# Performance work log

Measured on AMD Instinct MI355X. Metric: run time of the kernel, lower is better.

The kernel has to match this reference:

```python
import jax, jax.numpy as jnp
import numpy as np

N = 50000
E = 500000
C = 128
NUM_TYPES = 32
DIM_TOK = 94
STEPS = 3
BLOCKS = 2
NUM_ET = 3
LN_EPS = 1e-5


def setup_inputs() -> dict:
    key = jax.random.key(0)
    ks = jax.random.split(key, 16)
    s = 0.05
    return {
        "x_type": jax.random.randint(ks[0], (N,), 0, NUM_TYPES),
        "x_tok": jax.random.randint(ks[1], (N,), 0, DIM_TOK),
        "x_small": jax.random.normal(ks[2], (N, 2), jnp.float32),
        "edge_index": jax.random.randint(ks[3], (2, E), 0, N),
        "edge_type": jax.random.randint(ks[4], (E,), 0, NUM_ET),
        "conv_w": jax.random.normal(ks[5], (BLOCKS, NUM_ET, STEPS, C, C), jnp.float32) * s,
        "gru_wih": jax.random.normal(ks[6], (BLOCKS, NUM_ET, 3 * C, C), jnp.float32) * s,
        "gru_whh": jax.random.normal(ks[7], (BLOCKS, NUM_ET, 3 * C, C), jnp.float32) * s,
        "gru_bih": jnp.zeros((BLOCKS, NUM_ET, 3 * C), jnp.float32),
        "gru_bhh": jnp.zeros((BLOCKS, NUM_ET, 3 * C), jnp.float32),
        "ln_g": jnp.ones((BLOCKS, C), jnp.float32),
        "ln_b": jnp.zeros((BLOCKS, C), jnp.float32),
        "head_w1": jax.random.normal(ks[8], (C, C), jnp.float32) * s,
        "head_b1": jnp.zeros((C,), jnp.float32),
        "head_w2": jax.random.normal(ks[9], (2, C), jnp.float32) * s,
        "head_b2": jnp.zeros((2,), jnp.float32),
    }


def _gru_cell(x, h, wih, whh, bih, bhh):
    # torch.nn.GRUCell: gates ordered (r, z, n)
    gi = x @ wih.T + bih  # [N, 3C]
    gh = h @ whh.T + bhh
    gi_r, gi_z, gi_n = jnp.split(gi, 3, axis=-1)
    gh_r, gh_z, gh_n = jnp.split(gh, 3, axis=-1)
    r = jax.nn.sigmoid(gi_r + gh_r)
    z = jax.nn.sigmoid(gi_z + gh_z)
    n = jnp.tanh(gi_n + r * gh_n)
    return (1.0 - z) * n + z * h


def _forward(x_small, conv_w, gru_wih, gru_whh, gru_bih, gru_bhh, ln_g, ln_b,
             head_w1, head_b1, head_w2, head_b2, x_type, x_tok, edge_index, edge_type):
    # build_features: one-hot type, one-hot (clamped) token, small feats
    h_type = jax.nn.one_hot(x_type, NUM_TYPES, dtype=x_small.dtype)
    h_tok = jax.nn.one_hot(jnp.clip(x_tok, 0, DIM_TOK - 1), DIM_TOK, dtype=x_small.dtype)
    h = jnp.concatenate([h_type, h_tok, x_small], axis=1)  # [N, C]

    src, dst = edge_index[0], edge_index[1]

    for b in range(BLOCKS):
        total = jnp.zeros_like(h)
        for t in range(NUM_ET):
            # edge-type masking implemented as weighted scatter-add (sum aggr)
            em = (edge_type == t).astype(h.dtype)[:, None]  # [E, 1]
            m = h
            for s in range(STEPS):
                x = m @ conv_w[b, t, s]                     # [N, C]
                agg = jax.ops.segment_sum(x[src] * em, dst, num_segments=N)
                m = _gru_cell(agg, m,
                              gru_wih[b, t], gru_whh[b, t],
                              gru_bih[b, t], gru_bhh[b, t])
            total = total + m
        # LayerNorm(residual) + ReLU; dropout=0 (eval)
        hr = h + total
        mu = jnp.mean(hr, axis=-1, keepdims=True)
        var = jnp.var(hr, axis=-1, keepdims=True)
        h = (hr - mu) * jax.lax.rsqrt(var + LN_EPS) * ln_g[b] + ln_b[b]
        h = jax.nn.relu(h)

    # head applied per-node (module returns head(h), not head(pooled))
    z = jax.nn.relu(h @ head_w1.T + head_b1)
    return z @ head_w2.T + head_b2  # [N, 2]


def reference(x_type, x_tok, x_small, edge_index, edge_type, conv_w, gru_wih, gru_whh,
              gru_bih, gru_bhh, ln_g, ln_b, head_w1, head_b1, head_w2, head_b2):
    return _forward(x_small, conv_w, gru_wih, gru_whh, gru_bih, gru_bhh, ln_g, ln_b,
                    head_w1, head_b1, head_w2, head_b2, x_type, x_tok, edge_index, edge_type)
```

## Files before the change

kernel.cpp:

```cpp
#include <hip/hip_runtime.h>
#include <cstdint>
#include <cstddef>

#define N_NODES 50000
#define N_EDGES 500000
#define NB 782
#define NT 150000
#define NCHUNK2 586
#define FS 49152
#define PSTR 136
#define MAXOFF 12799744u
#define ECAP 1024

typedef _Float16 half8 __attribute__((ext_vector_type(8)));
typedef _Float16 half2v __attribute__((ext_vector_type(2)));
typedef float floatx4 __attribute__((ext_vector_type(4)));

__device__ __forceinline__ float sigmoid_(float x) { return 1.f / (1.f + __expf(-x)); }
__device__ __forceinline__ float tanh_(float x) {
  float t = __expf(-2.f * fabsf(x));
  float r = (1.f - t) / (1.f + t);
  return copysignf(r, x);
}

__global__ __launch_bounds__(256) void k_feat_hist(_Float16* __restrict__ h,
    const int* __restrict__ xtype, const int* __restrict__ xtok,
    const float* __restrict__ xs, const int* __restrict__ ei,
    const int* __restrict__ et, int* __restrict__ counts) {
  int idx = blockIdx.x * 256 + threadIdx.x;
  if (idx < N_NODES * 128) {
    int n = idx >> 7, c = idx & 127;
    float v;
    if (c < 32) {
      v = (xtype[n] == c) ? 1.f : 0.f;
    } else if (c < 126) {
      int tk = xtok[n];
      tk = tk < 0 ? 0 : (tk > 93 ? 93 : tk);
      v = (tk == (c - 32)) ? 1.f : 0.f;
    } else {
      v = xs[n * 2 + (c - 126)];
    }
    h[idx] = (_Float16)v;
  }
  if (idx < N_EDGES) {
    int d = ei[N_EDGES + idx];
    int ty = et[idx] & 3;
    if ((unsigned)d < N_NODES && ty < 3) atomicAdd(&counts[ty * N_NODES + d], 1);
  }
}

__global__ __launch_bounds__(256) void k_scan_a(const int* __restrict__ counts,
    int* __restrict__ bsum) {
  int i = blockIdx.x * 256 + threadIdx.x;
  int v = (i < NT) ? counts[i] : 0;
  int lane = threadIdx.x & 63, wv = threadIdx.x >> 6;
#pragma unroll
  for (int off = 32; off > 0; off >>= 1) v += __shfl_xor(v, off);
  __shared__ int ws[4];
  if (lane == 0) ws[wv] = v;
  __syncthreads();
  if (threadIdx.x == 0) bsum[blockIdx.x] = ws[0] + ws[1] + ws[2] + ws[3];
}

__global__ __launch_bounds__(256) void k_scan_c(const int* __restrict__ counts,
    const int* __restrict__ bsum, int* __restrict__ ptr, int* __restrict__ fill) {
  __shared__ int wsum2[4];
  __shared__ int ws[4];
  int lane = threadIdx.x & 63, wv = threadIdx.x >> 6;
  int acc = 0;
  for (int j = threadIdx.x; j < blockIdx.x; j += 256) acc += bsum[j];
#pragma unroll
  for (int off = 32; off > 0; off >>= 1) acc += __shfl_xor(acc, off);
  if (lane == 0) wsum2[wv] = acc;
  __syncthreads();
  int boffset = wsum2[0] + wsum2[1] + wsum2[2] + wsum2[3];
  int i = blockIdx.x * 256 + threadIdx.x;
  int v = (i < NT) ? counts[i] : 0;
  int s = v;
#pragma unroll
  for (int off = 1; off < 64; off <<= 1) { int u = __shfl_up(s, off); if (lane >= off) s += u; }
  if (lane == 63) ws[wv] = s;
  __syncthreads();
  int woff = 0;
#pragma unroll
  for (int w = 0; w < 4; ++w) woff += (w < wv) ? ws[w] : 0;
  int excl = boffset + woff + s - v;
  if (i < NT) { ptr[i] = excl; fill[i] = excl; }
  if (blockIdx.x == NCHUNK2 - 1 && threadIdx.x == 0)
    ptr[NT] = boffset + bsum[NCHUNK2 - 1];
}

__global__ __launch_bounds__(256) void k_place(const int* __restrict__ ei,
    const int* __restrict__ et, int* __restrict__ fill, int* __restrict__ csr) {
  int e = blockIdx.x * 256 + threadIdx.x;
  if (e >= N_EDGES) return;
  int srcv = ei[e], d = ei[N_EDGES + e], ty = et[e] & 3;
  if ((unsigned)d >= N_NODES || (unsigned)srcv >= N_NODES || ty >= 3) return;
  int pos = atomicAdd(&fill[ty * N_NODES + d], 1);
  if ((unsigned)pos < N_EDGES) csr[pos] = srcv << 8;
}

#define PREP_B (6 * 4 * 24 * 512)
#define PREP_MISC_BLOCKS ((PREP_B + 16384 + 511) / 512)
__global__ __launch_bounds__(512) void k_prep(const float* __restrict__ cw,
    const float* __restrict__ wih, const float* __restrict__ whh,
    const float* __restrict__ hw1, _Float16* __restrict__ dcomb,
    _Float16* __restrict__ dwhh, _Float16* __restrict__ dw1) {
  if (blockIdx.x < 36) {
    int mat = blockIdx.x >> 1, half = blockIdx.x & 1;
    int bt = mat / 3;
    int u = threadIdx.x >> 6, lane = threadIdx.x & 63;
    int quad = lane >> 4, l16 = lane & 15;
    floatx4 zero = {0.f, 0.f, 0.f, 0.f};
    floatx4 acc[4][3];
#pragma unroll
    for (int rt = 0; rt < 4; ++rt)
#pragma unroll
      for (int cc = 0; cc < 3; ++cc) acc[rt][cc] = zero;
#pragma unroll
    for (int jc = 0; jc < 4; ++jc) {
      half8 af[4], bf[3];
#pragma unroll
      for (int rt = 0; rt < 4; ++rt) {
        int m = half * 64 + rt * 16 + l16;
        const float* ap = cw + ((size_t)mat * 128 + m) * 128 + jc * 32 + quad * 8;
        floatx4 a0 = *(const floatx4*)ap;
        floatx4 a1 = *(const floatx4*)(ap + 4);
#pragma unroll
        for (int i = 0; i < 4; ++i) { af[rt][i] = (_Float16)a0[i]; af[rt][4 + i] = (_Float16)a1[i]; }
      }
#pragma unroll
      for (int cc = 0; cc < 3; ++cc) {
        int n = (u * 3 + cc) * 16 + l16;
        const float* bp = wih + ((size_t)bt * 384 + n) * 128 + jc * 32 + quad * 8;
        floatx4 b0 = *(const floatx4*)bp;
        floatx4 b1 = *(const floatx4*)(bp + 4);
#pragma unroll
        for (int i = 0; i < 4; ++i) { bf[cc][i] = (_Float16)b0[i]; bf[cc][4 + i] = (_Float16)b1[i]; }
      }
#pragma unroll
      for (int rt = 0; rt < 4; ++rt)
#pragma unroll
        for (int cc = 0; cc < 3; ++cc)
          acc[rt][cc] = __builtin_amdgcn_mfma_f32_16x16x32_f16(af[rt], bf[cc], acc[rt][cc], 0, 0, 0);
    }
#pragma unroll
    for (int rt = 0; rt < 4; ++rt) {
#pragma unroll
      for (int cc = 0; cc < 3; ++cc) {
        int ctg = u * 3 + cc;
#pragma unroll
        for (int q = 0; q < 4; ++q) {
          int k = half * 64 + rt * 16 + quad * 4 + q;
          int kc2 = k >> 5, r5 = k & 31;
          int lane2 = (r5 >> 3) * 16 + l16, j2 = r5 & 7;
          dcomb[(size_t)mat * FS + (size_t)((kc2 * 24 + ctg) * 64 + lane2) * 8 + j2] =
              (_Float16)acc[rt][cc][q];
        }
      }
    }
  } else {
    int idx0 = (blockIdx.x - 36) * 512 + threadIdx.x;
    if (idx0 < PREP_B) {
      int idx = idx0;
      int j = idx & 7, lane = (idx >> 3) & 63;
      int r = idx >> 9;
      int ct = r % 24;
      int r2 = r / 24;
      int kc = r2 & 3, bt = r2 >> 2;
      int k = kc * 32 + ((lane >> 4) & 3) * 8 + j;
      int n = ct * 16 + (lane & 15);
      dwhh[idx] = (_Float16)whh[((size_t)bt * 384 + n) * 128 + k];
    } else if (idx0 < PREP_B + 16384) {
      int idx = idx0 - PREP_B;
      int j = idx & 7, lane = (idx >> 3) & 63, ct = (idx >> 9) & 7, kc = (idx >> 12) & 3;
      int k = kc * 32 + ((lane >> 4) & 3) * 8 + j;
      int n = ct * 16 + (lane & 15);
      dw1[idx] = (_Float16)hw1[n * 128 + k];
    }
  }
}

__global__ __launch_bounds__(512, 4) void k_step(
    const _Float16* __restrict__ Mbase, const size_t mstride,
    _Float16* __restrict__ Sout,
    const int* __restrict__ ptr, const int* __restrict__ csr,
    const _Float16* __restrict__ WPC, const _Float16* __restrict__ WHH,
    const float* __restrict__ bi2, const float* __restrict__ bh2) {
  __shared__ __attribute__((aligned(16))) _Float16 Plds[64 * PSTR];
  __shared__ __attribute__((aligned(16))) _Float16 Mlds[64 * PSTR];
  __shared__ int Elds[ECAP];
  __shared__ int Pt[65];
  int bid = blockIdx.x;
  int t = bid / NB, blk = bid - t * NB;
  int tid = threadIdx.x;
  int wave = tid >> 6, lane = tid & 63;
  int quad = lane >> 4, l16 = lane & 15;
  int rowbase = blk * 64;
  const size_t NC = (size_t)N_NODES * 128;
  const _Float16* Mp = Mbase + mstride * t;
  const char* Mb = (const char*)Mp;
  _Float16* Sp = Sout + (size_t)t * NC;
  const int* ptrT = ptr + t * N_NODES;

  int rb64 = rowbase + 64; if (rb64 > N_NODES) rb64 = N_NODES;
  int bse = ptrT[rowbase];
  int cend = ptrT[rb64];
  if (bse < 0) bse = 0; if (bse > N_EDGES) bse = N_EDGES;
  if (cend < bse) cend = bse; if (cend > N_EDGES) cend = N_EDGES;
  int cnt = cend - bse; if (cnt > ECAP) cnt = ECAP;

  if (tid < 65) {
    int n = rowbase + tid; if (n > N_NODES) n = N_NODES;
    int v = ptrT[n] - bse;
    if (v < 0) v = 0; if (v > cnt) v = cnt;
    Pt[tid] = v;
  }
#pragma unroll
  for (int it = 0; it < 2; ++it) {
    int r = it * 32 + (tid >> 4);
    int c = (tid & 15) * 8;
    int gr = rowbase + r; if (gr >= N_NODES) gr = N_NODES - 1;
    half8 v = *(const half8*)(Mp + (size_t)gr * 128 + c);
    *(half8*)(&Mlds[r * PSTR + c]) = v;
  }
  for (int i = tid; i < cnt; i += 512) {
    unsigned off = (unsigned)csr[bse + i];
    if (off > MAXOFF) off = 0;
    Elds[i] = (int)off;
  }
  __syncthreads();

  int g = quad;
  unsigned coff = (unsigned)(l16 * 16);
  int nlA = wave * 8 + g, nlB = nlA + 4;
  int iA = Pt[nlA], eA = Pt[nlA + 1];
  int iB = Pt[nlB], eB = Pt[nlB + 1];
  half8 accA = {}, accB = {};
  while (__any(iA < eA || iB < eB)) {
#pragma unroll
    for (int uu = 0; uu < 4; ++uu) {
      if (iA + uu < eA) {
        unsigned o = (unsigned)Elds[iA + uu] + coff;
        accA += *(const half8*)(Mb + o);
      }
      if (iB + uu < eB) {
        unsigned o = (unsigned)Elds[iB + uu] + coff;
        accB += *(const half8*)(Mb + o);
      }
    }
    iA += 4; iB += 4;
  }
  *(half8*)(&Plds[nlA * PSTR + l16 * 8]) = accA;
  *(half8*)(&Plds[nlB * PSTR + l16 * 8]) = accB;
  __syncthreads();

  const half8* wpc = (const half8*)(WPC + (size_t)t * 3 * FS);
  const half8* whh = (const half8*)(WHH + (size_t)t * FS);
  const float* bi = bi2 + (size_t)t * 384;
  const float* bh = bh2 + (size_t)t * 384;
  int u = wave;
  floatx4 zero = {0.f, 0.f, 0.f, 0.f};
  floatx4 aR[4], aZ[4], aNP[4], aNM[4];
#pragma unroll
  for (int rt = 0; rt < 4; ++rt) { aR[rt] = zero; aZ[rt] = zero; aNP[rt] = zero; aNM[rt] = zero; }
#pragma unroll
  for (int kc = 0; kc < 4; ++kc) {
    half8 af[4];
#pragma unroll
    for (int rt = 0; rt < 4; ++rt)
      af[rt] = *(const half8*)(&Plds[(rt * 16 + l16) * PSTR + kc * 32 + quad * 8]);
    half8 br = wpc[(kc * 24 + u) * 64 + lane];
    half8 bz = wpc[(kc * 24 + 8 + u) * 64 + lane];
    half8 bn = wpc[(kc * 24 + 16 + u) * 64 + lane];
#pragma unroll
    for (int rt = 0; rt < 4; ++rt) {
      aR[rt] = __builtin_amdgcn_mfma_f32_16x16x32_f16(af[rt], br, aR[rt], 0, 0, 0);
      aZ[rt] = __builtin_amdgcn_mfma_f32_16x16x32_f16(af[rt], bz, aZ[rt], 0, 0, 0);
      aNP[rt] = __builtin_amdgcn_mfma_f32_16x16x32_f16(af[rt], bn, aNP[rt], 0, 0, 0);
    }
  }
#pragma unroll
  for (int kc = 0; kc < 4; ++kc) {
    half8 af[4];
#pragma unroll
    for (int rt = 0; rt < 4; ++rt)
      af[rt] = *(const half8*)(&Mlds[(rt * 16 + l16) * PSTR + kc * 32 + quad * 8]);
    half8 br = whh[(kc * 24 + u) * 64 + lane];
    half8 bz = whh[(kc * 24 + 8 + u) * 64 + lane];
    half8 bn = whh[(kc * 24 + 16 + u) * 64 + lane];
#pragma unroll
    for (int rt = 0; rt < 4; ++rt) {
      aR[rt] = __builtin_amdgcn_mfma_f32_16x16x32_f16(af[rt], br, aR[rt], 0, 0, 0);
      aZ[rt] = __builtin_amdgcn_mfma_f32_16x16x32_f16(af[rt], bz, aZ[rt], 0, 0, 0);
      aNM[rt] = __builtin_amdgcn_mfma_f32_16x16x32_f16(af[rt], bn, aNM[rt], 0, 0, 0);
    }
  }
  __syncthreads();
  int col = u * 16 + l16;
  float br_ = bi[col] + bh[col];
  float bz_ = bi[128 + col] + bh[128 + col];
  float bin = bi[256 + col], bhn = bh[256 + col];
#pragma unroll
  for (int rt = 0; rt < 4; ++rt) {
#pragma unroll
    for (int q = 0; q < 4; ++q) {
      int lr = rt * 16 + quad * 4 + q;
      float r = sigmoid_(aR[rt][q] + br_);
      float z = sigmoid_(aZ[rt][q] + bz_);
      float nt = tanh_(aNP[rt][q] + bin + r * (aNM[rt][q] + bhn));
      float hold = (float)Mlds[lr * PSTR + col];
      Plds[lr * PSTR + col] = (_Float16)((1.f - z) * nt + z * hold);
    }
  }
  __syncthreads();
#pragma unroll
  for (int it = 0; it < 2; ++it) {
    int r = it * 32 + (tid >> 4);
    int c = (tid & 15) * 8;
    int row = rowbase + r;
    if (row < N_NODES)
      *(half8*)(Sp + (size_t)row * 128 + c) = *(const half8*)(&Plds[r * PSTR + c]);
  }
}

__global__ __launch_bounds__(256) void k_ln16(_Float16* __restrict__ h,
    const _Float16* __restrict__ S, const float* __restrict__ gamma,
    const float* __restrict__ beta) {
  int wave = threadIdx.x >> 6, lane = threadIdx.x & 63;
  int g = lane >> 4, l16 = lane & 15;
  int row = blockIdx.x * 16 + wave * 4 + g;
  if (row >= N_NODES) return;
  const size_t NC = (size_t)N_NODES * 128;
  size_t base = (size_t)row * 128 + l16 * 8;
  half8 hv = *(const half8*)(h + base);
  half8 s0 = *(const half8*)(S + base);
  half8 s1 = *(const half8*)(S + NC + base);
  half8 s2 = *(const half8*)(S + 2 * NC + base);
  float v[8];
  float s = 0.f, sq = 0.f;
#pragma unroll
  for (int i = 0; i < 8; ++i) {
    v[i] = (float)hv[i] + (float)s0[i] + (float)s1[i] + (float)s2[i];
    s += v[i]; sq += v[i] * v[i];
  }
#pragma unroll
  for (int off = 1; off < 16; off <<= 1) {
    s += __shfl_xor(s, off);
    sq += __shfl_xor(sq, off);
  }
  float mu = s * 0.0078125f;
  float var = sq * 0.0078125f - mu * mu;
  float rs = rsqrtf(var + 1e-5f);
  half8 ov;
#pragma unroll
  for (int i = 0; i < 8; ++i) {
    float o = (v[i] - mu) * rs * gamma[l16 * 8 + i] + beta[l16 * 8 + i];
    ov[i] = (_Float16)fmaxf(o, 0.f);
  }
  *(half8*)(h + base) = ov;
}

__global__ __launch_bounds__(256, 4) void k_head(const _Float16* __restrict__ h,
    const _Float16* __restrict__ S, const float* __restrict__ gamma,
    const float* __restrict__ beta, const _Float16* __restrict__ Wf,
    const float* __restrict__ bias, const float* __restrict__ w2,
    const float* __restrict__ b2, float* __restrict__ out) {
  __shared__ __attribute__((aligned(16))) _Float16 zA[64 * PSTR];
  __shared__ __attribute__((aligned(16))) _Float16 zB[64 * PSTR];
  __shared__ float w2s[256];
  int wave = threadIdx.x >> 6, lane = threadIdx.x & 63;
  int quad = lane >> 4, l16 = lane & 15;
  int rowbase = blockIdx.x * 64;
  const size_t NC = (size_t)N_NODES * 128;
  w2s[threadIdx.x] = w2[threadIdx.x];
#pragma unroll
  for (int pass = 0; pass < 4; ++pass) {
    int rl = pass * 16 + wave * 4 + quad;
    int row = rowbase + rl; if (row >= N_NODES) row = N_NODES - 1;
    size_t base = (size_t)row * 128 + l16 * 8;
    half8 hv = *(const half8*)(h + base);
    half8 s0 = *(const half8*)(S + base);
    half8 s1 = *(const half8*)(S + NC + base);
    half8 s2 = *(const half8*)(S + 2 * NC + base);
    float v[8];
    float s = 0.f, sq = 0.f;
#pragma unroll
    for (int i = 0; i < 8; ++i) {
      v[i] = (float)hv[i] + (float)s0[i] + (float)s1[i] + (float)s2[i];
      s += v[i]; sq += v[i] * v[i];
    }
#pragma unroll
    for (int off = 1; off < 16; off <<= 1) {
      s += __shfl_xor(s, off);
      sq += __shfl_xor(sq, off);
    }
    float mu = s * 0.0078125f;
    float var = sq * 0.0078125f - mu * mu;
    float rs = rsqrtf(var + 1e-5f);
    half8 ov;
#pragma unroll
    for (int i = 0; i < 8; ++i) {
      float o = (v[i] - mu) * rs * gamma[l16 * 8 + i] + beta[l16 * 8 + i];
      ov[i] = (_Float16)fmaxf(o, 0.f);
    }
    *(half8*)(&zA[rl * PSTR + l16 * 8]) = ov;
  }
  __syncthreads();
  const half8* wf = (const half8*)Wf;
  floatx4 zero = {0.f, 0.f, 0.f, 0.f};
  floatx4 acc[4][2];
#pragma unroll
  for (int rt = 0; rt < 4; ++rt) { acc[rt][0] = zero; acc[rt][1] = zero; }
#pragma unroll
  for (int kc = 0; kc < 4; ++kc) {
    half8 af[4];
#pragma unroll
    for (int rt = 0; rt < 4; ++rt)
      af[rt] = *(const half8*)(&zA[(rt * 16 + l16) * PSTR + kc * 32 + quad * 8]);
    half8 b0 = wf[(kc * 8 + 2 * wave) * 64 + lane];
    half8 b1 = wf[(kc * 8 + 2 * wave + 1) * 64 + lane];
#pragma unroll
    for (int rt = 0; rt < 4; ++rt) {
      acc[rt][0] = __builtin_amdgcn_mfma_f32_16x16x32_f16(af[rt], b0, acc[rt][0], 0, 0, 0);
      acc[rt][1] = __builtin_amdgcn_mfma_f32_16x16x32_f16(af[rt], b1, acc[rt][1], 0, 0, 0);
    }
  }
  int col = wave * 32 + l16;
#pragma unroll
  for (int rt = 0; rt < 4; ++rt) {
#pragma unroll
    for (int q = 0; q < 4; ++q) {
      int lr = rt * 16 + quad * 4 + q;
      zB[lr * PSTR + col] = (_Float16)fmaxf(acc[rt][0][q] + bias[col], 0.f);
      zB[lr * PSTR + col + 16] = (_Float16)fmaxf(acc[rt][1][q] + bias[col + 16], 0.f);
    }
  }
  __syncthreads();
  int tid = threadIdx.x;
  if (tid < 128) {
    int lr = tid >> 1, o = tid & 1;
    int row = rowbase + lr;
    if (row < N_NODES) {
      const float* wr = w2s + o * 128;
      float a = 0.f;
#pragma unroll
      for (int k = 0; k < 128; ++k) a += (float)zB[lr * PSTR + k] * wr[k];
      out[(size_t)row * 2 + o] = a + b2[o];
    }
  }
}

extern "C" void kernel_launch(void* const* d_in, const int* in_sizes, int n_in,
                              void* d_out, int out_size, void* d_ws, size_t ws_size,
                              hipStream_t stream) {
  const int*   x_type  = (const int*)d_in[0];
  const int*   x_tok   = (const int*)d_in[1];
  const float* x_small = (const float*)d_in[2];
  const int*   eidx    = (const int*)d_in[3];
  const int*   etype   = (const int*)d_in[4];
  const float* conv_w  = (const float*)d_in[5];
  const float* gwih    = (const float*)d_in[6];
  const float* gwhh    = (const float*)d_in[7];
  const float* gbih    = (const float*)d_in[8];
  const float* gbhh    = (const float*)d_in[9];
  const float* ln_g    = (const float*)d_in[10];
  const float* ln_b    = (const float*)d_in[11];
  const float* hw1     = (const float*)d_in[12];
  const float* hb1     = (const float*)d_in[13];
  const float* hw2     = (const float*)d_in[14];
  const float* hb2     = (const float*)d_in[15];
  float* out = (float*)d_out;

  const size_t NC = (size_t)N_NODES * 128;
  char* W = (char*)d_ws;
  size_t off = 0;
  _Float16* h16 = (_Float16*)(W + off);     off += NC * 2;
  _Float16* S0  = (_Float16*)(W + off);     off += 3 * NC * 2;
  _Float16* S1  = (_Float16*)(W + off);     off += 3 * NC * 2;
  int* counts = (int*)(W + off);            off += (size_t)NT * 4;
  int* ptrv   = (int*)(W + off);            off += (size_t)(NT + 1) * 4;
  int* fill   = (int*)(W + off);            off += (size_t)NT * 4;
  int* bsum   = (int*)(W + off);            off += (NCHUNK2 + 1) * 4;
  int* csr    = (int*)(W + off);            off += (size_t)N_EDGES * 4;
  _Float16* WPC = (_Float16*)(W + off);     off += (size_t)18 * FS * 2;
  _Float16* WHH = (_Float16*)(W + off);     off += (size_t)6 * FS * 2;
  _Float16* W1F = (_Float16*)(W + off);     off += (size_t)16384 * 2;

  hipMemsetAsync(counts, 0, (size_t)NT * 4, stream);
  k_feat_hist<<<(N_NODES * 128 + 255) / 256, 256, 0, stream>>>(
      h16, x_type, x_tok, x_small, eidx, etype, counts);
  k_scan_a<<<NCHUNK2, 256, 0, stream>>>(counts, bsum);
  k_scan_c<<<NCHUNK2, 256, 0, stream>>>(counts, bsum, ptrv, fill);
  k_place<<<(N_EDGES + 255) / 256, 256, 0, stream>>>(eidx, etype, fill, csr);
  k_prep<<<36 + PREP_MISC_BLOCKS, 512, 0, stream>>>(
      conv_w, gwih, gwhh, hw1, WPC, WHH, W1F);

  for (int b = 0; b < 2; ++b) {
    for (int s = 0; s < 3; ++s) {
      const _Float16* Msrc = (s == 0) ? h16 : ((s == 1) ? S0 : S1);
      size_t mstr = (s == 0) ? 0 : NC;
      _Float16* Sout = (s == 1) ? S1 : S0;
      k_step<<<3 * NB, 512, 0, stream>>>(Msrc, mstr, Sout, ptrv, csr,
          WPC + (size_t)(b * 9 + s) * FS, WHH + (size_t)b * 3 * FS,
          gbih + (size_t)b * 3 * 384, gbhh + (size_t)b * 3 * 384);
    }
    if (b == 0)
      k_ln16<<<(N_NODES + 15) / 16, 256, 0, stream>>>(h16, S0, ln_g, ln_b);
  }
  k_head<<<NB, 256, 0, stream>>>(h16, S0, ln_g + 128, ln_b + 128,
                                 W1F, hb1, hw2, hb2, out);
}
```

Measured before the change: 673.1 us.

## Fuse LayerNorm and head into last GRU step via last-block-done counters

The final step kernel of each block now uses a per-row-tile atomic counter so that the last of the three edge-type blocks to finish a 64-row tile performs the LayerNorm (block 0) or LayerNorm plus MLP head (block 1) for that tile. This removes two separate kernel launches and their reads of h and the three S buffers from a cold pass, overlapping the epilogue with other tiles' step work. It adds threadfences, atomics and a memset of counters, and duplicates the step kernel code.

```diff
diff --git a/kernel.cpp b/kernel.cpp
--- a/kernel.cpp
+++ b/kernel.cpp
@@ -180,6 +180,7 @@
     }
   }
 }
+
 
 __global__ __launch_bounds__(512, 4) void k_step(
     const _Float16* __restrict__ Mbase, const size_t mstride,
@@ -324,129 +325,424 @@
   }
 }
 
-__global__ __launch_bounds__(256) void k_ln16(_Float16* __restrict__ h,
-    const _Float16* __restrict__ S, const float* __restrict__ gamma,
-    const float* __restrict__ beta) {
-  int wave = threadIdx.x >> 6, lane = threadIdx.x & 63;
-  int g = lane >> 4, l16 = lane & 15;
-  int row = blockIdx.x * 16 + wave * 4 + g;
-  if (row >= N_NODES) return;
+__global__ __launch_bounds__(512, 4) void k_step_ln(
+    const _Float16* __restrict__ Mbase, const size_t mstride,
+    _Float16* __restrict__ Sout,
+    const int* __restrict__ ptr, const int* __restrict__ csr,
+    const _Float16* __restrict__ WPC, const _Float16* __restrict__ WHH,
+    const float* __restrict__ bi2, const float* __restrict__ bh2,
+    _Float16* __restrict__ hbuf, const float* __restrict__ gamma,
+    const float* __restrict__ beta, int* __restrict__ fincnt) {
+  __shared__ __attribute__((aligned(16))) _Float16 Plds[64 * PSTR];
+  __shared__ __attribute__((aligned(16))) _Float16 Mlds[64 * PSTR];
+  __shared__ int Elds[ECAP];
+  __shared__ int Pt[65];
+  __shared__ int dofin;
+  int bid = blockIdx.x;
+  int t = bid / NB, blk = bid - t * NB;
+  int tid = threadIdx.x;
+  int wave = tid >> 6, lane = tid & 63;
+  int quad = lane >> 4, l16 = lane & 15;
+  int rowbase = blk * 64;
   const size_t NC = (size_t)N_NODES * 128;
-  size_t base = (size_t)row * 128 + l16 * 8;
-  half8 hv = *(const half8*)(h + base);
-  half8 s0 = *(const half8*)(S + base);
-  half8 s1 = *(const half8*)(S + NC + base);
-  half8 s2 = *(const half8*)(S + 2 * NC + base);
-  float v[8];
-  float s = 0.f, sq = 0.f;
-#pragma unroll
-  for (int i = 0; i < 8; ++i) {
-    v[i] = (float)hv[i] + (float)s0[i] + (float)s1[i] + (float)s2[i];
-    s += v[i]; sq += v[i] * v[i];
-  }
-#pragma unroll
-  for (int off = 1; off < 16; off <<= 1) {
-    s += __shfl_xor(s, off);
-    sq += __shfl_xor(sq, off);
-  }
-  float mu = s * 0.0078125f;
-  float var = sq * 0.0078125f - mu * mu;
-  float rs = rsqrtf(var + 1e-5f);
-  half8 ov;
-#pragma unroll
-  for (int i = 0; i < 8; ++i) {
-    float o = (v[i] - mu) * rs * gamma[l16 * 8 + i] + beta[l16 * 8 + i];
-    ov[i] = (_Float16)fmaxf(o, 0.f);
-  }
-  *(half8*)(h + base) = ov;
-}
-
-__global__ __launch_bounds__(256, 4) void k_head(const _Float16* __restrict__ h,
-    const _Float16* __restrict__ S, const float* __restrict__ gamma,
-    const float* __restrict__ beta, const _Float16* __restrict__ Wf,
-    const float* __restrict__ bias, const float* __restrict__ w2,
-    const float* __restrict__ b2, float* __restrict__ out) {
-  __shared__ __attribute__((aligned(16))) _Float16 zA[64 * PSTR];
-  __shared__ __attribute__((aligned(16))) _Float16 zB[64 * PSTR];
-  __shared__ float w2s[256];
-  int wave = threadIdx.x >> 6, lane = threadIdx.x & 63;
-  int quad = lane >> 4, l16 = lane & 15;
-  int rowbase = blockIdx.x * 64;
-  const size_t NC = (size_t)N_NODES * 128;
-  w2s[threadIdx.x] = w2[threadIdx.x];
-#pragma unroll
-  for (int pass = 0; pass < 4; ++pass) {
-    int rl = pass * 16 + wave * 4 + quad;
-    int row = rowbase + rl; if (row >= N_NODES) row = N_NODES - 1;
-    size_t base = (size_t)row * 128 + l16 * 8;
-    half8 hv = *(const half8*)(h + base);
-    half8 s0 = *(const half8*)(S + base);
-    half8 s1 = *(const half8*)(S + NC + base);
-    half8 s2 = *(const half8*)(S + 2 * NC + base);
-    float v[8];
-    float s = 0.f, sq = 0.f;
-#pragma unroll
-    for (int i = 0; i < 8; ++i) {
-      v[i] = (float)hv[i] + (float)s0[i] + (float)s1[i] + (float)s2[i];
-      s += v[i]; sq += v[i] * v[i];
-    }
-#pragma unroll
-    for (int off = 1; off < 16; off <<= 1) {
-      s += __shfl_xor(s, off);
-      sq += __shfl_xor(sq, off);
-    }
-    float mu = s * 0.0078125f;
-    float var = sq * 0.0078125f - mu * mu;
-    float rs = rsqrtf(var + 1e-5f);
-    half8 ov;
-#pragma unroll
-    for (int i = 0; i < 8; ++i) {
-      float o = (v[i] - mu) * rs * gamma[l16 * 8 + i] + beta[l16 * 8 + i];
-      ov[i] = (_Float16)fmaxf(o, 0.f);
-    }
-    *(half8*)(&zA[rl * PSTR + l16 * 8]) = ov;
-  }
-  __syncthreads();
-  const half8* wf = (const half8*)Wf;
+  const _Float16* Mp = Mbase + mstride * t;
+  const char* Mb = (const char*)Mp;
+  _Float16* Sp = Sout + (size_t)t * NC;
+  const int* ptrT = ptr + t * N_NODES;
+
+  int rb64 = rowbase + 64; if (rb64 > N_NODES) rb64 = N_NODES;
+  int bse = ptrT[rowbase];
+  int cend = ptrT[rb64];
+  if (bse < 0) bse = 0; if (bse > N_EDGES) bse = N_EDGES;
+  if (cend < bse) cend = bse; if (cend > N_EDGES) cend = N_EDGES;
+  int cnt = cend - bse; if (cnt > ECAP) cnt = ECAP;
+
+  if (tid < 65) {
+    int n = rowbase + tid; if (n > N_NODES) n = N_NODES;
+    int v = ptrT[n] - bse;
+    if (v < 0) v = 0; if (v > cnt) v = cnt;
+    Pt[tid] = v;
+  }
+#pragma unroll
+  for (int it = 0; it < 2; ++it) {
+    int r = it * 32 + (tid >> 4);
+    int c = (tid & 15) * 8;
+    int gr = rowbase + r; if (gr >= N_NODES) gr = N_NODES - 1;
+    half8 v = *(const half8*)(Mp + (size_t)gr * 128 + c);
+    *(half8*)(&Mlds[r * PSTR + c]) = v;
+  }
+  for (int i = tid; i < cnt; i += 512) {
+    unsigned off = (unsigned)csr[bse + i];
+    if (off > MAXOFF) off = 0;
+    Elds[i] = (int)off;
+  }
+  __syncthreads();
+
+  int g = quad;
+  unsigned coff = (unsigned)(l16 * 16);
+  int nlA = wave * 8 + g, nlB = nlA + 4;
+  int iA = Pt[nlA], eA = Pt[nlA + 1];
+  int iB = Pt[nlB], eB = Pt[nlB + 1];
+  half8 accA = {}, accB = {};
+  while (__any(iA < eA || iB < eB)) {
+#pragma unroll
+    for (int uu = 0; uu < 4; ++uu) {
+      if (iA + uu < eA) {
+        unsigned o = (unsigned)Elds[iA + uu] + coff;
+        accA += *(const half8*)(Mb + o);
+      }
+      if (iB + uu < eB) {
+        unsigned o = (unsigned)Elds[iB + uu] + coff;
+        accB += *(const half8*)(Mb + o);
+      }
+    }
+    iA += 4; iB += 4;
+  }
+  *(half8*)(&Plds[nlA * PSTR + l16 * 8]) = accA;
+  *(half8*)(&Plds[nlB * PSTR + l16 * 8]) = accB;
+  __syncthreads();
+
+  const half8* wpc = (const half8*)(WPC + (size_t)t * 3 * FS);
+  const half8* whh = (const half8*)(WHH + (size_t)t * FS);
+  const float* bi = bi2 + (size_t)t * 384;
+  const float* bh = bh2 + (size_t)t * 384;
+  int u = wave;
   floatx4 zero = {0.f, 0.f, 0.f, 0.f};
-  floatx4 acc[4][2];
-#pragma unroll
-  for (int rt = 0; rt < 4; ++rt) { acc[rt][0] = zero; acc[rt][1] = zero; }
+  floatx4 aR[4], aZ[4], aNP[4], aNM[4];
+#pragma unroll
+  for (int rt = 0; rt < 4; ++rt) { aR[rt] = zero; aZ[rt] = zero; aNP[rt] = zero; aNM[rt] = zero; }
 #pragma unroll
   for (int kc = 0; kc < 4; ++kc) {
     half8 af[4];
 #pragma unroll
     for (int rt = 0; rt < 4; ++rt)
-      af[rt] = *(const half8*)(&zA[(rt * 16 + l16) * PSTR + kc * 32 + quad * 8]);
-    half8 b0 = wf[(kc * 8 + 2 * wave) * 64 + lane];
-    half8 b1 = wf[(kc * 8 + 2 * wave + 1) * 64 + lane];
+      af[rt] = *(const half8*)(&Plds[(rt * 16 + l16) * PSTR + kc * 32 + quad * 8]);
+    half8 br = wpc[(kc * 24 + u) * 64 + lane];
+    half8 bz = wpc[(kc * 24 + 8 + u) * 64 + lane];
+    half8 bn = wpc[(kc * 24 + 16 + u) * 64 + lane];
 #pragma unroll
     for (int rt = 0; rt < 4; ++rt) {
-      acc[rt][0] = __builtin_amdgcn_mfma_f32_16x16x32_f16(af[rt], b0, acc[rt][0], 0, 0, 0);
-      acc[rt][1] = __builtin_amdgcn_mfma_f32_16x16x32_f16(af[rt], b1, acc[rt][1], 0, 0, 0);
-    }
-  }
-  int col = wave * 32 + l16;
+      aR[rt] = __builtin_amdgcn_mfma_f32_16x16x32_f16(af[rt], br, aR[rt], 0, 0, 0);
+      aZ[rt] = __builtin_amdgcn_mfma_f32_16x16x32_f16(af[rt], bz, aZ[rt], 0, 0, 0);
+      aNP[rt] = __builtin_amdgcn_mfma_f32_16x16x32_f16(af[rt], bn, aNP[rt], 0, 0, 0);
+    }
+  }
+#pragma unroll
+  for (int kc = 0; kc < 4; ++kc) {
+    half8 af[4];
+#pragma unroll
+    for (int rt = 0; rt < 4; ++rt)
+      af[rt] = *(const half8*)(&Mlds[(rt * 16 + l16) * PSTR + kc * 32 + quad * 8]);
+    half8 br = whh[(kc * 24 + u) * 64 + lane];
+    half8 bz = whh[(kc * 24 + 8 + u) * 64 + lane];
+    half8 bn = whh[(kc * 24 + 16 + u) * 64 + lane];
+#pragma unroll
+    for (int rt = 0; rt < 4; ++rt) {
+      aR[rt] = __builtin_amdgcn_mfma_f32_16x16x32_f16(af[rt], br, aR[rt], 0, 0, 0);
+      aZ[rt] = __builtin_amdgcn_mfma_f32_16x16x32_f16(af[rt], bz, aZ[rt], 0, 0, 0);
+      aNM[rt] = __builtin_amdgcn_mfma_f32_16x16x32_f16(af[rt], bn, aNM[rt], 0, 0, 0);
+    }
+  }
+  __syncthreads();
+  int col = u * 16 + l16;
+  float br_ = bi[col] + bh[col];
+  float bz_ = bi[128 + col] + bh[128 + col];
+  float bin = bi[256 + col], bhn = bh[256 + col];
 #pragma unroll
   for (int rt = 0; rt < 4; ++rt) {
 #pragma unroll
     for (int q = 0; q < 4; ++q) {
       int lr = rt * 16 + quad * 4 + q;
-      zB[lr * PSTR + col] = (_Float16)fmaxf(acc[rt][0][q] + bias[col], 0.f);
-      zB[lr * PSTR + col + 16] = (_Float16)fmaxf(acc[rt][1][q] + bias[col + 16], 0.f);
-    }
-  }
-  __syncthreads();
+      float r = sigmoid_(aR[rt][q] + br_);
+      float z = sigmoid_(aZ[rt][q] + bz_);
+      float nt = tanh_(aNP[rt][q] + bin + r * (aNM[rt][q] + bhn));
+      float hold = (float)Mlds[lr * PSTR + col];
+      Plds[lr * PSTR + col] = (_Float16)((1.f - z) * nt + z * hold);
+    }
+  }
+  __syncthreads();
+#pragma unroll
+  for (int it = 0; it < 2; ++it) {
+    int r = it * 32 + (tid >> 4);
+    int c = (tid & 15) * 8;
+    int row = rowbase + r;
+    if (row < N_NODES)
+      *(half8*)(Sp + (size_t)row * 128 + c) = *(const half8*)(&Plds[r * PSTR + c]);
+  }
+  __threadfence();
+  __syncthreads();
+  if (tid == 0) dofin = (atomicAdd(&fincnt[blk], 1) == 2) ? 1 : 0;
+  __syncthreads();
+  if (dofin) {
+    __threadfence();
+    int l16b = tid & 15;
+#pragma unroll
+    for (int pass = 0; pass < 2; ++pass) {
+      int rl = pass * 32 + (tid >> 4);
+      int row = rowbase + rl;
+      int rowc = row < N_NODES ? row : N_NODES - 1;
+      size_t base = (size_t)rowc * 128 + l16b * 8;
+      half8 hv = *(const half8*)(hbuf + base);
+      half8 s0 = *(const half8*)(Sout + base);
+      half8 s1 = *(const half8*)(Sout + NC + base);
+      half8 s2 = *(const half8*)(Sout + 2 * NC + base);
+      float v[8];
+      float s = 0.f, sq = 0.f;
+#pragma unroll
+      for (int i = 0; i < 8; ++i) {
+        v[i] = (float)hv[i] + (float)s0[i] + (float)s1[i] + (float)s2[i];
+        s += v[i]; sq += v[i] * v[i];
+      }
+#pragma unroll
+      for (int off = 1; off < 16; off <<= 1) {
+        s += __shfl_xor(s, off);
+        sq += __shfl_xor(sq, off);
+      }
+      float mu = s * 0.0078125f;
+      float var = sq * 0.0078125f - mu * mu;
+      float rs = rsqrtf(var + 1e-5f);
+      half8 ov;
+#pragma unroll
+      for (int i = 0; i < 8; ++i) {
+        float o = (v[i] - mu) * rs * gamma[l16b * 8 + i] + beta[l16b * 8 + i];
+        ov[i] = (_Float16)fmaxf(o, 0.f);
+      }
+      if (row < N_NODES) *(half8*)(hbuf + base) = ov;
+    }
+  }
+}
+
+__global__ __launch_bounds__(512, 4) void k_step_hd(
+    const _Float16* __restrict__ Mbase, const size_t mstride,
+    _Float16* __restrict__ Sout,
+    const int* __restrict__ ptr, const int* __restrict__ csr,
+    const _Float16* __restrict__ WPC, const _Float16* __restrict__ WHH,
+    const float* __restrict__ bi2, const float* __restrict__ bh2,
+    const _Float16* __restrict__ hbuf, const float* __restrict__ gamma,
+    const float* __restrict__ beta, int* __restrict__ fincnt,
+    const _Float16* __restrict__ W1f, const float* __restrict__ hb1,
+    const float* __restrict__ w2, const float* __restrict__ b2,
+    float* __restrict__ out) {
+  __shared__ __attribute__((aligned(16))) _Float16 Plds[64 * PSTR];
+  __shared__ __attribute__((aligned(16))) _Float16 Mlds[64 * PSTR];
+  __shared__ int Elds[ECAP];
+  __shared__ int Pt[65];
+  __shared__ int dofin;
+  int bid = blockIdx.x;
+  int t = bid / NB, blk = bid - t * NB;
   int tid = threadIdx.x;
-  if (tid < 128) {
-    int lr = tid >> 1, o = tid & 1;
-    int row = rowbase + lr;
-    if (row < N_NODES) {
-      const float* wr = w2s + o * 128;
-      float a = 0.f;
-#pragma unroll
-      for (int k = 0; k < 128; ++k) a += (float)zB[lr * PSTR + k] * wr[k];
-      out[(size_t)row * 2 + o] = a + b2[o];
+  int wave = tid >> 6, lane = tid & 63;
+  int quad = lane >> 4, l16 = lane & 15;
+  int rowbase = blk * 64;
+  const size_t NC = (size_t)N_NODES * 128;
+  const _Float16* Mp = Mbase + mstride * t;
+  const char* Mb = (const char*)Mp;
+  _Float16* Sp = Sout + (size_t)t * NC;
+  const int* ptrT = ptr + t * N_NODES;
+
+  int rb64 = rowbase + 64; if (rb64 > N_NODES) rb64 = N_NODES;
+  int bse = ptrT[rowbase];
+  int cend = ptrT[rb64];
+  if (bse < 0) bse = 0; if (bse > N_EDGES) bse = N_EDGES;
+  if (cend < bse) cend = bse; if (cend > N_EDGES) cend = N_EDGES;
+  int cnt = cend - bse; if (cnt > ECAP) cnt = ECAP;
+
+  if (tid < 65) {
+    int n = rowbase + tid; if (n > N_NODES) n = N_NODES;
+    int v = ptrT[n] - bse;
+    if (v < 0) v = 0; if (v > cnt) v = cnt;
+    Pt[tid] = v;
+  }
+#pragma unroll
+  for (int it = 0; it < 2; ++it) {
+    int r = it * 32 + (tid >> 4);
+    int c = (tid & 15) * 8;
+    int gr = rowbase + r; if (gr >= N_NODES) gr = N_NODES - 1;
+    half8 v = *(const half8*)(Mp + (size_t)gr * 128 + c);
+    *(half8*)(&Mlds[r * PSTR + c]) = v;
+  }
+  for (int i = tid; i < cnt; i += 512) {
+    unsigned off = (unsigned)csr[bse + i];
+    if (off > MAXOFF) off = 0;
+    Elds[i] = (int)off;
+  }
+  __syncthreads();
+
+  int g = quad;
+  unsigned coff = (unsigned)(l16 * 16);
+  int nlA = wave * 8 + g, nlB = nlA + 4;
+  int iA = Pt[nlA], eA = Pt[nlA + 1];
+  int iB = Pt[nlB], eB = Pt[nlB + 1];
+  half8 accA = {}, accB = {};
+  while (__any(iA < eA || iB < eB)) {
+#pragma unroll
+    for (int uu = 0; uu < 4; ++uu) {
+      if (iA + uu < eA) {
+        unsigned o = (unsigned)Elds[iA + uu] + coff;
+        accA += *(const half8*)(Mb + o);
+      }
+      if (iB + uu < eB) {
+        unsigned o = (unsigned)Elds[iB + uu] + coff;
+        accB += *(const half8*)(Mb + o);
+      }
+    }
+    iA += 4; iB += 4;
+  }
+  *(half8*)(&Plds[nlA * PSTR + l16 * 8]) = accA;
+  *(half8*)(&Plds[nlB * PSTR + l16 * 8]) = accB;
+  __syncthreads();
+
+  const half8* wpc = (const half8*)(WPC + (size_t)t * 3 * FS);
+  const half8* whh = (const half8*)(WHH + (size_t)t * FS);
+  const float* bi = bi2 + (size_t)t * 384;
+  const float* bh = bh2 + (size_t)t * 384;
+  int u = wave;
+  floatx4 zero = {0.f, 0.f, 0.f, 0.f};
+  floatx4 aR[4], aZ[4], aNP[4], aNM[4];
+#pragma unroll
+  for (int rt = 0; rt < 4; ++rt) { aR[rt] = zero; aZ[rt] = zero; aNP[rt] = zero; aNM[rt] = zero; }
+#pragma unroll
+  for (int kc = 0; kc < 4; ++kc) {
+    half8 af[4];
+#pragma unroll
+    for (int rt = 0; rt < 4; ++rt)
+      af[rt] = *(const half8*)(&Plds[(rt * 16 + l16) * PSTR + kc * 32 + quad * 8]);
+    half8 br = wpc[(kc * 24 + u) * 64 + lane];
+    half8 bz = wpc[(kc * 24 + 8 + u) * 64 + lane];
+    half8 bn = wpc[(kc * 24 + 16 + u) * 64 + lane];
+#pragma unroll
+    for (int rt = 0; rt < 4; ++rt) {
+      aR[rt] = __builtin_amdgcn_mfma_f32_16x16x32_f16(af[rt], br, aR[rt], 0, 0, 0);
+      aZ[rt] = __builtin_amdgcn_mfma_f32_16x16x32_f16(af[rt], bz, aZ[rt], 0, 0, 0);
+      aNP[rt] = __builtin_amdgcn_mfma_f32_16x16x32_f16(af[rt], bn, aNP[rt], 0, 0, 0);
+    }
+  }
+#pragma unroll
+  for (int kc = 0; kc < 4; ++kc) {
+    half8 af[4];
+#pragma unroll
+    for (int rt = 0; rt < 4; ++rt)
+      af[rt] = *(const half8*)(&Mlds[(rt * 16 + l16) * PSTR + kc * 32 + quad * 8]);
+    half8 br = whh[(kc * 24 + u) * 64 + lane];
+    half8 bz = whh[(kc * 24 + 8 + u) * 64 + lane];
+    half8 bn = whh[(kc * 24 + 16 + u) * 64 + lane];
+#pragma unroll
+    for (int rt = 0; rt < 4; ++rt) {
+      aR[rt] = __builtin_amdgcn_mfma_f32_16x16x32_f16(af[rt], br, aR[rt], 0, 0, 0);
+      aZ[rt] = __builtin_amdgcn_mfma_f32_16x16x32_f16(af[rt], bz, aZ[rt], 0, 0, 0);
+      aNM[rt] = __builtin_amdgcn_mfma_f32_16x16x32_f16(af[rt], bn, aNM[rt], 0, 0, 0);
+    }
+  }
+  __syncthreads();
+  int col = u * 16 + l16;
+  float br_ = bi[col] + bh[col];
+  float bz_ = bi[128 + col] + bh[128 + col];
+  float bin = bi[256 + col], bhn = bh[256 + col];
+#pragma unroll
+  for (int rt = 0; rt < 4; ++rt) {
+#pragma unroll
+    for (int q = 0; q < 4; ++q) {
+      int lr = rt * 16 + quad * 4 + q;
+      float r = sigmoid_(aR[rt][q] + br_);
+      float z = sigmoid_(aZ[rt][q] + bz_);
+      float nt = tanh_(aNP[rt][q] + bin + r * (aNM[rt][q] + bhn));
+      float hold = (float)Mlds[lr * PSTR + col];
+      Plds[lr * PSTR + col] = (_Float16)((1.f - z) * nt + z * hold);
+    }
+  }
+  __syncthreads();
+#pragma unroll
+  for (int it = 0; it < 2; ++it) {
+    int r = it * 32 + (tid >> 4);
+    int c = (tid & 15) * 8;
+    int row = rowbase + r;
+    if (row < N_NODES)
+      *(half8*)(Sp + (size_t)row * 128 + c) = *(const half8*)(&Plds[r * PSTR + c]);
+  }
+  __threadfence();
+  __syncthreads();
+  if (tid == 0) dofin = (atomicAdd(&fincnt[blk], 1) == 2) ? 1 : 0;
+  __syncthreads();
+  if (dofin) {
+    __threadfence();
+    float* w2s = (float*)Elds;
+    if (tid < 256) w2s[tid] = w2[tid];
+    int l16b = tid & 15;
+#pragma unroll
+    for (int pass = 0; pass < 2; ++pass) {
+      int rl = pass * 32 + (tid >> 4);
+      int row = rowbase + rl;
+      int rowc = row < N_NODES ? row : N_NODES - 1;
+      size_t base = (size_t)rowc * 128 + l16b * 8;
+      half8 hv = *(const half8*)(hbuf + base);
+      half8 s0 = *(const half8*)(Sout + base);
+      half8 s1 = *(const half8*)(Sout + NC + base);
+      half8 s2 = *(const half8*)(Sout + 2 * NC + base);
+      float v[8];
+      float s = 0.f, sq = 0.f;
+#pragma unroll
+      for (int i = 0; i < 8; ++i) {
+        v[i] = (float)hv[i] + (float)s0[i] + (float)s1[i] + (float)s2[i];
+        s += v[i]; sq += v[i] * v[i];
+      }
+#pragma unroll
+      for (int off = 1; off < 16; off <<= 1) {
+        s += __shfl_xor(s, off);
+        sq += __shfl_xor(sq, off);
+      }
+      float mu = s * 0.0078125f;
+      float var = sq * 0.0078125f - mu * mu;
+      float rs = rsqrtf(var + 1e-5f);
+      half8 ov;
+#pragma unroll
+      for (int i = 0; i < 8; ++i) {
+        float o = (v[i] - mu) * rs * gamma[l16b * 8 + i] + beta[l16b * 8 + i];
+        ov[i] = (_Float16)fmaxf(o, 0.f);
+      }
+      *(half8*)(&Plds[rl * PSTR + l16b * 8]) = ov;
+    }
+    __syncthreads();
+    if (wave < 4) {
+      const half8* wf = (const half8*)W1f;
+      floatx4 hacc[4][2];
+#pragma unroll
+      for (int rt = 0; rt < 4; ++rt) { hacc[rt][0] = zero; hacc[rt][1] = zero; }
+#pragma unroll
+      for (int kc = 0; kc < 4; ++kc) {
+        half8 af[4];
+#pragma unroll
+        for (int rt = 0; rt < 4; ++rt)
+          af[rt] = *(const half8*)(&Plds[(rt * 16 + l16) * PSTR + kc * 32 + quad * 8]);
+        half8 b0 = wf[(kc * 8 + 2 * wave) * 64 + lane];
+        half8 b1 = wf[(kc * 8 + 2 * wave + 1) * 64 + lane];
+#pragma unroll
+        for (int rt = 0; rt < 4; ++rt) {
+          hacc[rt][0] = __builtin_amdgcn_mfma_f32_16x16x32_f16(af[rt], b0, hacc[rt][0], 0, 0, 0);
+          hacc[rt][1] = __builtin_amdgcn_mfma_f32_16x16x32_f16(af[rt], b1, hacc[rt][1], 0, 0, 0);
+        }
+      }
+      int hcol = wave * 32 + l16;
+#pragma unroll
+      for (int rt = 0; rt < 4; ++rt) {
+#pragma unroll
+        for (int q = 0; q < 4; ++q) {
+          int lr = rt * 16 + quad * 4 + q;
+          Mlds[lr * PSTR + hcol] = (_Float16)fmaxf(hacc[rt][0][q] + hb1[hcol], 0.f);
+          Mlds[lr * PSTR + hcol + 16] = (_Float16)fmaxf(hacc[rt][1][q] + hb1[hcol + 16], 0.f);
+        }
+      }
+    }
+    __syncthreads();
+    if (tid < 128) {
+      int lr = tid >> 1, o = tid & 1;
+      int row = rowbase + lr;
+      if (row < N_NODES) {
+        const float* wr = w2s + o * 128;
+        float a = 0.f;
+#pragma unroll
+        for (int k = 0; k < 128; ++k) a += (float)Mlds[lr * PSTR + k] * wr[k];
+        out[(size_t)row * 2 + o] = a + b2[o];
+      }
     }
   }
 }
@@ -479,6 +775,8 @@
   _Float16* S0  = (_Float16*)(W + off);     off += 3 * NC * 2;
   _Float16* S1  = (_Float16*)(W + off);     off += 3 * NC * 2;
   int* counts = (int*)(W + off);            off += (size_t)NT * 4;
+  int* lncnt  = (int*)(W + off);            off += 1024 * 4;
+  int* hdcnt  = (int*)(W + off);            off += 1024 * 4;
   int* ptrv   = (int*)(W + off);            off += (size_t)(NT + 1) * 4;
   int* fill   = (int*)(W + off);            off += (size_t)NT * 4;
   int* bsum   = (int*)(W + off);            off += (NCHUNK2 + 1) * 4;
@@ -487,7 +785,7 @@
   _Float16* WHH = (_Float16*)(W + off);     off += (size_t)6 * FS * 2;
   _Float16* W1F = (_Float16*)(W + off);     off += (size_t)16384 * 2;
 
-  hipMemsetAsync(counts, 0, (size_t)NT * 4, stream);
+  hipMemsetAsync(counts, 0, ((size_t)NT + 2048) * 4, stream);
   k_feat_hist<<<(N_NODES * 128 + 255) / 256, 256, 0, stream>>>(
       h16, x_type, x_tok, x_small, eidx, etype, counts);
   k_scan_a<<<NCHUNK2, 256, 0, stream>>>(counts, bsum);
@@ -501,13 +799,23 @@
       const _Float16* Msrc = (s == 0) ? h16 : ((s == 1) ? S0 : S1);
       size_t mstr = (s == 0) ? 0 : NC;
       _Float16* Sout = (s == 1) ? S1 : S0;
-      k_step<<<3 * NB, 512, 0, stream>>>(Msrc, mstr, Sout, ptrv, csr,
-          WPC + (size_t)(b * 9 + s) * FS, WHH + (size_t)b * 3 * FS,
-          gbih + (size_t)b * 3 * 384, gbhh + (size_t)b * 3 * 384);
-    }
-    if (b == 0)
-      k_ln16<<<(N_NODES + 15) / 16, 256, 0, stream>>>(h16, S0, ln_g, ln_b);
-  }
-  k_head<<<NB, 256, 0, stream>>>(h16, S0, ln_g + 128, ln_b + 128,
-                                 W1F, hb1, hw2, hb2, out);
-}
+      const _Float16* WPCb = WPC + (size_t)(b * 9 + s) * FS;
+      const _Float16* WHHb = WHH + (size_t)b * 3 * FS;
+      const float* bib = gbih + (size_t)b * 3 * 384;
+      const float* bhb = gbhh + (size_t)b * 3 * 384;
+      if (s < 2) {
+        k_step<<<3 * NB, 512, 0, stream>>>(Msrc, mstr, Sout, ptrv, csr,
+                                           WPCb, WHHb, bib, bhb);
+      } else if (b == 0) {
+        k_step_ln<<<3 * NB, 512, 0, stream>>>(Msrc, mstr, Sout, ptrv, csr,
+                                              WPCb, WHHb, bib, bhb,
+                                              h16, ln_g, ln_b, lncnt);
+      } else {
+        k_step_hd<<<3 * NB, 512, 0, stream>>>(Msrc, mstr, Sout, ptrv, csr,
+                                              WPCb, WHHb, bib, bhb,
+                                              h16, ln_g + 128, ln_b + 128, hdcnt,
+                                              W1F, hb1, hw2, hb2, out);
+      }
+    }
+  }
+}
```

Result: slower. 1.690 ms (+151.1%).
